# Performance work log

Hardware: AMD Instinct MI355X
Metric: run time of the kernel (lower is better)

Reference implementation:

```python
import jax, jax.numpy as jnp
import numpy as np

NVOC, NINPUT, NHID, NLAYERS = 32000, 512, 512, 2
SEQ, BATCH = 128, 32


def setup_inputs() -> dict:
    key = jax.random.key(0)
    ks = jax.random.split(key, 6)
    inp = jax.random.randint(ks[0], (SEQ, BATCH), 0, NVOC)
    # init_weights(): embed and decoder weight uniform(-0.1, 0.1), decoder bias zero
    embed_W = jax.random.uniform(ks[1], (NVOC, NINPUT), minval=-0.1, maxval=0.1, dtype=jnp.float32)
    # per-layer LSTM gate projections: Linear(nhid+ninput, 4*nhid) (ninput==nhid so stackable)
    fan_in = NHID + NINPUT
    bound = 1.0 / np.sqrt(fan_in)
    fc_W = jax.random.uniform(ks[2], (NLAYERS, 4 * NHID, fan_in), minval=-bound, maxval=bound, dtype=jnp.float32)
    fc_b = jax.random.uniform(ks[3], (NLAYERS, 4 * NHID), minval=-bound, maxval=bound, dtype=jnp.float32)
    dec_W = jax.random.uniform(ks[4], (NVOC, NHID), minval=-0.1, maxval=0.1, dtype=jnp.float32)
    dec_b = jnp.zeros((NVOC,), dtype=jnp.float32)
    return {"input": inp, "embed_W": embed_W, "fc_W": fc_W, "fc_b": fc_b,
            "dec_W": dec_W, "dec_b": dec_b}


def _lstm(emb, fc_W, fc_b):
    # emb: [S, B, ninput]; fc_W: [L, 4H, 2H]; returns output [S,B,H], hidden [L,B,H]
    B = emb.shape[1]
    h0 = jnp.zeros((NLAYERS, B, NHID), emb.dtype)
    c0 = jnp.zeros((NLAYERS, B, NHID), emb.dtype)

    def step(carry, x_t):
        h, c = carry
        inp = x_t  # layer-0 input for this timestep
        new_h, new_c = [], []
        for l in range(NLAYERS):
            a = jnp.concatenate([inp, h[l]], axis=-1) @ fc_W[l].T + fc_b[l]  # [B, 4H]
            i_g = jax.nn.sigmoid(a[:, :NHID])
            f_g = jax.nn.sigmoid(a[:, NHID:2 * NHID])
            o_g = jax.nn.sigmoid(a[:, 2 * NHID:3 * NHID])
            b_g = jnp.tanh(a[:, 3 * NHID:])
            c_l = f_g * c[l] + i_g * b_g
            h_l = o_g * jnp.tanh(c_l)
            new_h.append(h_l)
            new_c.append(c_l)
            inp = h_l
        h = jnp.stack(new_h)
        c = jnp.stack(new_c)
        return (h, c), h[-1]

    (h_fin, _), out = jax.lax.scan(step, (h0, c0), emb)
    return out, h_fin


def reference(input, embed_W, fc_W, fc_b, dec_W, dec_b):
    # Dropout is identity in eval mode; adversarial_training=False path.
    emb = embed_W[input]                       # [S, B, ninput]
    out, hidden = _lstm(emb, fc_W, fc_b)       # [S, B, H], [L, B, H]
    decoded = out @ dec_W.T + dec_b            # [S, B, nvoc]
    return decoded, hidden
```

## Files before the change

### kernel.cpp

```cpp
#include <hip/hip_runtime.h>
#include <stdint.h>

typedef unsigned short u16;
typedef __attribute__((ext_vector_type(8))) short short8;
typedef __attribute__((ext_vector_type(4))) short short4v;
typedef __attribute__((ext_vector_type(4))) float floatx4;

#define SEQ 128
#define BATCH 32
#define NHID 512
#define NVOC 32000
#define LSTM_WGS 64

__device__ __forceinline__ u16 f2bf(float f) {
  uint32_t u;
  __builtin_memcpy(&u, &f, 4);
  uint32_t r = (u + 0x7fffu + ((u >> 16) & 1u)) >> 16;
  return (u16)r;
}
__device__ __forceinline__ short8 cvt8(floatx4 a, floatx4 b) {
  short8 o;
  o[0] = (short)f2bf(a[0]); o[1] = (short)f2bf(a[1]);
  o[2] = (short)f2bf(a[2]); o[3] = (short)f2bf(a[3]);
  o[4] = (short)f2bf(b[0]); o[5] = (short)f2bf(b[1]);
  o[6] = (short)f2bf(b[2]); o[7] = (short)f2bf(b[3]);
  return o;
}

__device__ __forceinline__ void gload_lds16(const u16* g, u16* l) {
  __builtin_amdgcn_global_load_lds(
      (const __attribute__((address_space(1))) uint32_t*)g,
      (__attribute__((address_space(3))) uint32_t*)l, 16, 0, 0);
}

__global__ void embed_kernel(const int* __restrict__ tok, const float* __restrict__ embW,
                             u16* __restrict__ emb) {
  int row = blockIdx.x;
  int t = tok[row];
  const floatx4* s = (const floatx4*)(embW + (size_t)t * NHID);
  int i = threadIdx.x;
  floatx4 a = s[i * 2], b = s[i * 2 + 1];
  ((short8*)(emb + (size_t)row * NHID))[i] = cvt8(a, b);
}

__global__ void conv_bf16_kernel(const float* __restrict__ src, u16* __restrict__ dst) {
  int i = blockIdx.x * 256 + threadIdx.x;
  floatx4 v = ((const floatx4*)src)[i];
  short4v o;
  o[0] = (short)f2bf(v[0]); o[1] = (short)f2bf(v[1]);
  o[2] = (short)f2bf(v[2]); o[3] = (short)f2bf(v[3]);
  ((short4v*)dst)[i] = o;
}

__global__ __launch_bounds__(256, 1) void lstm_kernel(
    const u16* __restrict__ emb, const float* __restrict__ fcW, const float* __restrict__ fcb,
    u16* __restrict__ h0_all, u16* __restrict__ h1_all, float* __restrict__ hfin,
    int* __restrict__ bar) {
  const int tid  = threadIdx.x;
  const int wave = tid >> 6;
  const int lane = tid & 63;
  const int layer = wave >> 1;
  const int u0 = blockIdx.x * 8 + (wave & 1) * 4;
  const int q  = lane >> 4;
  const int ln = lane & 15;

  const int wrow = (ln & 3) * NHID + u0 + (ln >> 2);
  const float* WrowF = fcW + ((size_t)layer * 4 * NHID + (size_t)wrow) * (2 * NHID) + q * 8;
  short8 a_frag[32];
#pragma unroll
  for (int ks = 0; ks < 32; ks++) {
    floatx4 wa = *(const floatx4*)(WrowF + ks * 32);
    floatx4 wb = *(const floatx4*)(WrowF + ks * 32 + 4);
    a_frag[ks] = cvt8(wa, wb);
  }

  const int uc = u0 + q;
  float bias[4];
#pragma unroll
  for (int r = 0; r < 4; r++)
    bias[r] = fcb[layer * 4 * NHID + r * NHID + uc];

  float c_state[2] = {0.f, 0.f};

  for (int p = 0; p <= SEQ; p++) {
    const bool active = (layer == 0) ? (p < SEQ) : (p >= 1);
    if (active) {
      const int t = (layer == 0) ? p : p - 1;
      const u16* srcX = (layer == 0) ? (emb    + (size_t)t       * BATCH * NHID)
                                     : (h0_all + (size_t)(t + 1) * BATCH * NHID);
      const u16* srcH = (layer == 0) ? (h0_all + (size_t)t * BATCH * NHID)
                                     : (h1_all + (size_t)t * BATCH * NHID);
      floatx4 acc[2] = {{0.f,0.f,0.f,0.f},{0.f,0.f,0.f,0.f}};
#pragma unroll
      for (int ks = 0; ks < 16; ks++) {
#pragma unroll
        for (int bt = 0; bt < 2; bt++) {
          short8 bfrag = *(const short8*)(srcX + (size_t)(bt * 16 + ln) * NHID + ks * 32 + q * 8);
          acc[bt] = __builtin_amdgcn_mfma_f32_16x16x32_bf16(a_frag[ks], bfrag, acc[bt], 0, 0, 0);
        }
      }
#pragma unroll
      for (int ks = 16; ks < 32; ks++) {
#pragma unroll
        for (int bt = 0; bt < 2; bt++) {
          short8 bfrag = *(const short8*)(srcH + (size_t)(bt * 16 + ln) * NHID + (ks - 16) * 32 + q * 8);
          acc[bt] = __builtin_amdgcn_mfma_f32_16x16x32_bf16(a_frag[ks], bfrag, acc[bt], 0, 0, 0);
        }
      }
      u16* dst = ((layer == 0) ? h0_all : h1_all) + (size_t)(t + 1) * BATCH * NHID;
#pragma unroll
      for (int bt = 0; bt < 2; bt++) {
        float i_g = 1.f / (1.f + __expf(-(acc[bt][0] + bias[0])));
        float f_g = 1.f / (1.f + __expf(-(acc[bt][1] + bias[1])));
        float o_g = 1.f / (1.f + __expf(-(acc[bt][2] + bias[2])));
        float g_g = tanhf(acc[bt][3] + bias[3]);
        float cn  = f_g * c_state[bt] + i_g * g_g;
        c_state[bt] = cn;
        float h = o_g * tanhf(cn);
        dst[(size_t)(bt * 16 + ln) * NHID + uc] = f2bf(h);
        if (t == SEQ - 1)
          hfin[((size_t)layer * BATCH + bt * 16 + ln) * NHID + uc] = h;
      }
    }
    if (p < SEQ) {
      __syncthreads();
      if (tid == 0) {
        __hip_atomic_fetch_add(bar, 1, __ATOMIC_RELEASE, __HIP_MEMORY_SCOPE_AGENT);
        const int target = LSTM_WGS * (p + 1);
        while (__hip_atomic_load(bar, __ATOMIC_RELAXED, __HIP_MEMORY_SCOPE_AGENT) < target)
          __builtin_amdgcn_s_sleep(2);
        __builtin_amdgcn_fence(__ATOMIC_ACQUIRE, "agent");
      }
      __syncthreads();
    }
  }
}

__global__ __launch_bounds__(256) void dec_kernel(
    const u16* __restrict__ A, const u16* __restrict__ B,
    const float* __restrict__ bias, float* __restrict__ C) {
  __shared__ u16 lA[128 * 64];
  __shared__ u16 lB[128 * 64];
  const int tid  = threadIdx.x;
  const int wave = tid >> 6, lane = tid & 63;
  const int wm = wave >> 1, wn = wave & 1;
  const int q = lane >> 4, ln = lane & 15;
  const int mbase = blockIdx.x * 128;
  const int nbase = blockIdx.y * 128;

  floatx4 acc[4][4];
#pragma unroll
  for (int i = 0; i < 4; i++)
#pragma unroll
    for (int j = 0; j < 4; j++) acc[i][j] = (floatx4){0.f, 0.f, 0.f, 0.f};

  const int srow = tid >> 3;
  const int scol = (tid & 7) * 8;

  const u16* Ag = A + (size_t)mbase * 512;
  const u16* Bg = B + (size_t)nbase * 512;

  for (int kt = 0; kt < 8; kt++) {
#pragma unroll
    for (int it = 0; it < 4; it++) {
      const int row = it * 32 + srow;
      gload_lds16(Ag + (size_t)row * 512 + kt * 64 + scol, &lA[row * 64 + scol]);
      gload_lds16(Bg + (size_t)row * 512 + kt * 64 + scol, &lB[row * 64 + scol]);
    }
    asm volatile("s_waitcnt vmcnt(0)" ::: "memory");
    __syncthreads();
#pragma unroll
    for (int ks2 = 0; ks2 < 2; ks2++) {
      short8 af[4], bf[4];
#pragma unroll
      for (int i = 0; i < 4; i++) {
        af[i] = *(const short8*)&lA[(wm * 64 + i * 16 + ln) * 64 + ks2 * 32 + q * 8];
        bf[i] = *(const short8*)&lB[(wn * 64 + i * 16 + ln) * 64 + ks2 * 32 + q * 8];
      }
#pragma unroll
      for (int mt = 0; mt < 4; mt++)
#pragma unroll
        for (int nt = 0; nt < 4; nt++)
          acc[mt][nt] = __builtin_amdgcn_mfma_f32_16x16x32_bf16(af[mt], bf[nt], acc[mt][nt], 0, 0, 0);
    }
    __syncthreads();
  }

  const int mb2 = mbase + wm * 64;
  const int nb2 = nbase + wn * 64;
#pragma unroll
  for (int nt = 0; nt < 4; nt++) {
    const int col = nb2 + nt * 16 + ln;
    const float bv = bias[col];
#pragma unroll
    for (int mt = 0; mt < 4; mt++) {
      const int row0 = mb2 + mt * 16 + q * 4;
#pragma unroll
      for (int r = 0; r < 4; r++)
        C[(size_t)(row0 + r) * NVOC + col] = acc[mt][nt][r] + bv;
    }
  }
}

extern "C" void kernel_launch(void* const* d_in, const int* in_sizes, int n_in,
                              void* d_out, int out_size, void* d_ws, size_t ws_size,
                              hipStream_t stream) {
  const int*   tok  = (const int*)d_in[0];
  const float* embW = (const float*)d_in[1];
  const float* fcW  = (const float*)d_in[2];
  const float* fcb  = (const float*)d_in[3];
  const float* decW = (const float*)d_in[4];
  const float* decb = (const float*)d_in[5];
  float* out = (float*)d_out;

  char* ws = (char*)d_ws;
  const size_t embB = (size_t)SEQ * BATCH * NHID * 2;
  const size_t hB   = (size_t)(SEQ + 1) * BATCH * NHID * 2;
  const size_t decB = (size_t)NVOC * NHID * 2;
  u16* emb     = (u16*)ws;
  u16* h0_all  = (u16*)(ws + embB);
  u16* h1_all  = (u16*)(ws + embB + hB);
  u16* decWbf  = (u16*)(ws + embB + 2 * hB);
  int* bar     = (int*)(ws + embB + 2 * hB + decB);

  hipMemsetAsync(bar, 0, 256, stream);
  hipMemsetAsync(h0_all, 0, (size_t)BATCH * NHID * 2, stream);
  hipMemsetAsync(h1_all, 0, (size_t)BATCH * NHID * 2, stream);

  embed_kernel<<<SEQ * BATCH, 64, 0, stream>>>(tok, embW, emb);
  conv_bf16_kernel<<<(NVOC * NHID) / 1024, 256, 0, stream>>>(decW, decWbf);
  lstm_kernel<<<LSTM_WGS, 256, 0, stream>>>(emb, fcW, fcb, h0_all, h1_all,
                                            out + (size_t)SEQ * BATCH * NVOC, bar);
  dec_kernel<<<dim3((SEQ * BATCH) / 128, NVOC / 128), 256, 0, stream>>>(
      h1_all + (size_t)BATCH * NHID, decWbf, decb, out);
}
```

Measured before the change: 2.218 ms.

## Overlap LSTM input projection with grid barrier and double-buffer decoder LDS tiles

The LSTM loop now runs the input-side MFMAs (embedding or layer-0 output) before waiting on the grid-wide barrier, and only waits before the recurrent h-side half. The arrive and wait are split so each workgroup signals after writing h and spins at the start of the next step. The layer-1 schedule is delayed by two steps so its input is ready without waiting, at the cost of one extra pipeline step. Separately, the decoder GEMM double-buffers its LDS tiles, prefetching the next K slice while computing the current one, using raw s_barrier and partial vmcnt waits, which doubles LDS use per block.

```diff
diff --git a/kernel.cpp b/kernel.cpp
--- a/kernel.cpp
+++ b/kernel.cpp
@@ -82,15 +82,14 @@
 
   float c_state[2] = {0.f, 0.f};
 
-  for (int p = 0; p <= SEQ; p++) {
-    const bool active = (layer == 0) ? (p < SEQ) : (p >= 1);
-    if (active) {
-      const int t = (layer == 0) ? p : p - 1;
+  for (int p = 0; p <= SEQ + 1; p++) {
+    const int t = (layer == 0) ? p : p - 2;
+    const bool act = (t >= 0) && (t < SEQ);
+    floatx4 acc[2] = {{0.f,0.f,0.f,0.f},{0.f,0.f,0.f,0.f}};
+
+    if (act) {
       const u16* srcX = (layer == 0) ? (emb    + (size_t)t       * BATCH * NHID)
                                      : (h0_all + (size_t)(t + 1) * BATCH * NHID);
-      const u16* srcH = (layer == 0) ? (h0_all + (size_t)t * BATCH * NHID)
-                                     : (h1_all + (size_t)t * BATCH * NHID);
-      floatx4 acc[2] = {{0.f,0.f,0.f,0.f},{0.f,0.f,0.f,0.f}};
 #pragma unroll
       for (int ks = 0; ks < 16; ks++) {
 #pragma unroll
@@ -99,6 +98,21 @@
           acc[bt] = __builtin_amdgcn_mfma_f32_16x16x32_bf16(a_frag[ks], bfrag, acc[bt], 0, 0, 0);
         }
       }
+    }
+
+    if (p >= 1) {
+      if (tid == 0) {
+        const int target = LSTM_WGS * p;
+        while (__hip_atomic_load(bar, __ATOMIC_RELAXED, __HIP_MEMORY_SCOPE_AGENT) < target)
+          __builtin_amdgcn_s_sleep(2);
+        __builtin_amdgcn_fence(__ATOMIC_ACQUIRE, "agent");
+      }
+      __syncthreads();
+    }
+
+    if (act) {
+      const u16* srcH = (layer == 0) ? (h0_all + (size_t)t * BATCH * NHID)
+                                     : (h1_all + (size_t)t * BATCH * NHID);
 #pragma unroll
       for (int ks = 16; ks < 32; ks++) {
 #pragma unroll
@@ -122,16 +136,11 @@
           hfin[((size_t)layer * BATCH + bt * 16 + ln) * NHID + uc] = h;
       }
     }
-    if (p < SEQ) {
+
+    if (p <= SEQ) {
       __syncthreads();
-      if (tid == 0) {
+      if (tid == 0)
         __hip_atomic_fetch_add(bar, 1, __ATOMIC_RELEASE, __HIP_MEMORY_SCOPE_AGENT);
-        const int target = LSTM_WGS * (p + 1);
-        while (__hip_atomic_load(bar, __ATOMIC_RELAXED, __HIP_MEMORY_SCOPE_AGENT) < target)
-          __builtin_amdgcn_s_sleep(2);
-        __builtin_amdgcn_fence(__ATOMIC_ACQUIRE, "agent");
-      }
-      __syncthreads();
     }
   }
 }
@@ -139,8 +148,8 @@
 __global__ __launch_bounds__(256) void dec_kernel(
     const u16* __restrict__ A, const u16* __restrict__ B,
     const float* __restrict__ bias, float* __restrict__ C) {
-  __shared__ u16 lA[128 * 64];
-  __shared__ u16 lB[128 * 64];
+  __shared__ u16 lA[2][128 * 64];
+  __shared__ u16 lB[2][128 * 64];
   const int tid  = threadIdx.x;
   const int wave = tid >> 6, lane = tid & 63;
   const int wm = wave >> 1, wn = wave & 1;
@@ -160,22 +169,35 @@
   const u16* Ag = A + (size_t)mbase * 512;
   const u16* Bg = B + (size_t)nbase * 512;
 
+#pragma unroll
+  for (int it = 0; it < 4; it++) {
+    const int row = it * 32 + srow;
+    gload_lds16(Ag + (size_t)row * 512 + scol, &lA[0][row * 64 + scol]);
+    gload_lds16(Bg + (size_t)row * 512 + scol, &lB[0][row * 64 + scol]);
+  }
+
   for (int kt = 0; kt < 8; kt++) {
-#pragma unroll
-    for (int it = 0; it < 4; it++) {
-      const int row = it * 32 + srow;
-      gload_lds16(Ag + (size_t)row * 512 + kt * 64 + scol, &lA[row * 64 + scol]);
-      gload_lds16(Bg + (size_t)row * 512 + kt * 64 + scol, &lB[row * 64 + scol]);
-    }
-    asm volatile("s_waitcnt vmcnt(0)" ::: "memory");
-    __syncthreads();
+    const int cur = kt & 1;
+    if (kt < 7) {
+#pragma unroll
+      for (int it = 0; it < 4; it++) {
+        const int row = it * 32 + srow;
+        gload_lds16(Ag + (size_t)row * 512 + (kt + 1) * 64 + scol, &lA[cur ^ 1][row * 64 + scol]);
+        gload_lds16(Bg + (size_t)row * 512 + (kt + 1) * 64 + scol, &lB[cur ^ 1][row * 64 + scol]);
+      }
+      asm volatile("s_waitcnt vmcnt(8)" ::: "memory");
+    } else {
+      asm volatile("s_waitcnt vmcnt(0)" ::: "memory");
+    }
+    __builtin_amdgcn_s_barrier();
+    asm volatile("" ::: "memory");
 #pragma unroll
     for (int ks2 = 0; ks2 < 2; ks2++) {
       short8 af[4], bf[4];
 #pragma unroll
       for (int i = 0; i < 4; i++) {
-        af[i] = *(const short8*)&lA[(wm * 64 + i * 16 + ln) * 64 + ks2 * 32 + q * 8];
-        bf[i] = *(const short8*)&lB[(wn * 64 + i * 16 + ln) * 64 + ks2 * 32 + q * 8];
+        af[i] = *(const short8*)&lA[cur][(wm * 64 + i * 16 + ln) * 64 + ks2 * 32 + q * 8];
+        bf[i] = *(const short8*)&lB[cur][(wn * 64 + i * 16 + ln) * 64 + ks2 * 32 + q * 8];
       }
 #pragma unroll
       for (int mt = 0; mt < 4; mt++)
@@ -183,7 +205,8 @@
         for (int nt = 0; nt < 4; nt++)
           acc[mt][nt] = __builtin_amdgcn_mfma_f32_16x16x32_bf16(af[mt], bf[nt], acc[mt][nt], 0, 0, 0);
     }
-    __syncthreads();
+    asm volatile("" ::: "memory");
+    __builtin_amdgcn_s_barrier();
   }
 
   const int mb2 = mbase + wm * 64;
```

After: 2.089 ms. 5.8% less time.
